# Performance work log

Hardware: AMD Instinct MI355X
Metric: run time of the kernel (lower is better)

## Reference

```python
import jax, jax.numpy as jnp
import numpy as np

N_STK = 32
N_STK_PNT = 64
EMB = 512
BS = 32


def _layer(x, W, scale, bias):
    # Conv2d 1x1 (no bias) + folded BatchNorm2d (eval) + LeakyReLU(0.2)
    # x: [b, c_in, i, j], W: [c_out, c_in]
    h = jnp.einsum('oc,bcij->boij', W, x)
    h = h * scale[None, :, None, None] + bias[None, :, None, None]
    return jax.nn.leaky_relu(h, 0.2)


def setup_inputs() -> dict:
    key = jax.random.key(0)
    ks = jax.random.split(key, 14)
    std = 1.0 / np.sqrt(EMB)
    d = {
        'sparse_fea': jax.random.normal(ks[0], (BS, EMB, N_STK), jnp.float32),
        'dense_fea': jax.random.normal(ks[1], (BS, EMB, N_STK * N_STK_PNT), jnp.float32),
        'Wq': jax.random.normal(ks[2], (EMB, EMB), jnp.float32) * std,
        'sq': jnp.ones((EMB,), jnp.float32),
        'bq': jnp.zeros((EMB,), jnp.float32),
        'Wk': jax.random.normal(ks[3], (EMB, EMB), jnp.float32) * std,
        'sk': jnp.ones((EMB,), jnp.float32),
        'bk': jnp.zeros((EMB,), jnp.float32),
        'Wv': jax.random.normal(ks[4], (EMB, EMB), jnp.float32) * std,
        'sv': jnp.ones((EMB,), jnp.float32),
        'bv': jnp.zeros((EMB,), jnp.float32),
        'Wg': jax.random.normal(ks[5], (EMB, EMB), jnp.float32) * std,
        'sg': jnp.ones((EMB,), jnp.float32),
        'bg': jnp.zeros((EMB,), jnp.float32),
    }
    return d


def reference(sparse_fea, dense_fea, Wq, sq, bq, Wk, sk, bk, Wv, sv, bv, Wg, sg, bg):
    bs, emb, n_pnt = dense_fea.shape
    dense = dense_fea.reshape(bs, emb, N_STK, N_STK_PNT)     # [b, e, s, p]
    sparse = sparse_fea[:, :, :, None]                        # [b, e, s, 1]

    sp_q = _layer(sparse, Wq, sq, bq)                         # [b, E, s, 1]
    dn_k = _layer(dense, Wk, sk, bk)                          # [b, E, s, p]
    sp_v = _layer(sparse, Wv, sv, bv)                         # [b, E, s, 1]

    g = _layer(sp_q - dn_k, Wg, sg, bg)                       # [b, E, s, p]
    coef = jax.nn.softmax(g, axis=1)                          # channel softmax
    out = jnp.sum(coef * sp_v, axis=3)                        # [b, E, s]
    return out
```

## Files before the change

kernel.cpp:

```cpp
#include <hip/hip_runtime.h>
#include <hip/hip_bf16.h>

#define EMB 512
#define NSTK 32
#define NPNT 64
#define BSZ 32

typedef __attribute__((ext_vector_type(8))) _Float16 f16x8;
typedef __attribute__((ext_vector_type(4))) float f32x4;
typedef __attribute__((ext_vector_type(4))) unsigned short us4;
typedef __attribute__((ext_vector_type(8))) unsigned short us8;

static __device__ __forceinline__ unsigned short f16bits(float x) {
    _Float16 h = (_Float16)x;
    return *reinterpret_cast<unsigned short*>(&h);
}

#define GLL(gsrc, ldst)                                                         \
    __builtin_amdgcn_global_load_lds(                                           \
        (const __attribute__((address_space(1))) void*)(gsrc),                  \
        (__attribute__((address_space(3))) void*)(ldst), 16, 0, 0)

#define SBAR() __builtin_amdgcn_s_barrier()

__global__ __launch_bounds__(256)
void prep(const float* __restrict__ wk, const float* __restrict__ wg,
          _Float16* __restrict__ wkf, _Float16* __restrict__ wgf,
          const float* __restrict__ sparse,
          const float* __restrict__ Wq, const float* __restrict__ sq, const float* __restrict__ bq,
          const float* __restrict__ Wv, const float* __restrict__ sv, const float* __restrict__ bv,
          float* __restrict__ outq, float* __restrict__ outv) {
    if (blockIdx.x < 512) {
        int idx = blockIdx.x * blockDim.x + threadIdx.x;
        const float* src;
        _Float16* dst;
        int k;
        if (idx < 65536) { src = wk; dst = wkf; k = idx; }
        else             { src = wg; dst = wgf; k = idx - 65536; }
        f32x4 v = *reinterpret_cast<const f32x4*>(src + (size_t)k * 4);
        us4 o;
#pragma unroll
        for (int e = 0; e < 4; ++e) o[e] = f16bits(v[e]);
        *reinterpret_cast<us4*>(dst + (size_t)k * 4) = o;
        return;
    }

    const int bid = blockIdx.x - 512;
    const int bx = bid & 15, by = (bid >> 4) & 7, bz = bid >> 7;
    const float* W  = (bz == 0) ? Wq : Wv;
    const float* sc = (bz == 0) ? sq : sv;
    const float* bi = (bz == 0) ? bq : bv;
    float* orow     = (bz == 0) ? outq : outv;

    __shared__ float Wt[64][33];
    __shared__ float St[32][65];

    const int m0 = bx * 64;
    const int o0 = by * 64;
    const int t  = threadIdx.x;
    const int ty = t >> 4, tx = t & 15;

    float acc[4][4] = {};

    for (int k0 = 0; k0 < 512; k0 += 32) {
        {
            int ol = t >> 2, kl = (t & 3) * 8;
            const float* p = W + (size_t)(o0 + ol) * 512 + k0 + kl;
            f32x4 v0 = *reinterpret_cast<const f32x4*>(p);
            f32x4 v1 = *reinterpret_cast<const f32x4*>(p + 4);
#pragma unroll
            for (int e = 0; e < 4; ++e) { Wt[ol][kl + e] = v0[e]; Wt[ol][kl + 4 + e] = v1[e]; }
        }
        {
            int kl = t >> 3, ml = (t & 7) * 8;
            int mm = m0 + ml;
            int bb = mm >> 5, iidx = mm & 31;
            const float* p = sparse + (size_t)bb * 16384 + (size_t)(k0 + kl) * 32 + iidx;
            f32x4 v0 = *reinterpret_cast<const f32x4*>(p);
            f32x4 v1 = *reinterpret_cast<const f32x4*>(p + 4);
#pragma unroll
            for (int e = 0; e < 4; ++e) { St[kl][ml + e] = v0[e]; St[kl][ml + 4 + e] = v1[e]; }
        }
        __syncthreads();
#pragma unroll
        for (int kk = 0; kk < 32; ++kk) {
            float av[4], bvv[4];
#pragma unroll
            for (int e = 0; e < 4; ++e) av[e]  = Wt[ty * 4 + e][kk];
#pragma unroll
            for (int e = 0; e < 4; ++e) bvv[e] = St[kk][tx * 4 + e];
#pragma unroll
            for (int a = 0; a < 4; ++a)
#pragma unroll
                for (int bb2 = 0; bb2 < 4; ++bb2) acc[a][bb2] += av[a] * bvv[bb2];
        }
        __syncthreads();
    }
#pragma unroll
    for (int ae = 0; ae < 4; ++ae) {
        int o = o0 + ty * 4 + ae;
        float s = sc[o], bb2 = bi[o];
#pragma unroll
        for (int be = 0; be < 4; ++be) {
            int mm = m0 + tx * 4 + be;
            float h = acc[ae][be] * s + bb2;
            h = (h >= 0.f) ? h : 0.2f * h;
            orow[(size_t)mm * 512 + o] = h;
        }
    }
}

__global__ __launch_bounds__(1024, 4)
void fused_attn(const float* __restrict__ dense,
                const _Float16* __restrict__ wkf,
                const _Float16* __restrict__ wgf,
                const float* __restrict__ wsq,
                const float* __restrict__ wsv,
                const float* __restrict__ sk, const float* __restrict__ bk,
                const float* __restrict__ sg, const float* __restrict__ bg,
                float* __restrict__ out) {
    __shared__ __align__(16) _Float16 XH[64][520];
    __shared__ __align__(16) _Float16 WP[2][512 * 32];
    __shared__ __align__(16) float qrow[512];
    __shared__ __align__(16) float vrow[512];
    __shared__ float wredA[16][64];
    __shared__ float wredB[16][64];

    const int m   = blockIdx.x;
    const int b   = m >> 5, ii = m & 31;
    const int tid = threadIdx.x;
    const int w   = tid >> 6;
    const int l   = tid & 63;
    const int l15 = l & 15;
    const int lk  = l >> 4;

    const int tsw = ((l & 3) - ((l >> 3) & 3)) & 3;
    const int orl = l >> 2;

    {
#pragma unroll
        for (int ih = 0; ih < 2; ++ih) {
            const int o = w * 32 + ih * 16 + orl;
            GLL(wkf + (size_t)o * 512 + tsw * 8,
                &WP[0][(w * 32 + ih * 16) * 32]);
        }
    }

    if (tid < 512) qrow[tid] = wsq[(size_t)m * 512 + tid];
    else           vrow[tid - 512] = wsv[(size_t)m * 512 + (tid - 512)];

    {
        const float* src = dense + (size_t)b * 512 * 2048 + (size_t)ii * 64 + l;
#pragma unroll
        for (int e8 = 0; e8 < 4; ++e8) {
            const int c0 = w * 32 + e8 * 8;
            us8 pk;
#pragma unroll
            for (int e = 0; e < 8; ++e)
                pk[e] = f16bits(src[(size_t)(c0 + e) * 2048]);
            *reinterpret_cast<us8*>(&XH[l][c0]) = pk;
        }
    }
    __syncthreads();

    f32x4 acc[2][4];
#pragma unroll
    for (int fm = 0; fm < 2; ++fm)
#pragma unroll
        for (int fn = 0; fn < 4; ++fn) acc[fm][fn] = (f32x4){0.f, 0.f, 0.f, 0.f};

    const int aslot = (lk + ((l15 >> 1) & 3)) & 3;

    for (int ks = 0; ks < 16; ++ks) {
        {
            const _Float16* wsp = (ks < 15) ? (wkf + (size_t)(ks + 1) * 32) : wgf;
            _Float16* pb = WP[(ks + 1) & 1];
#pragma unroll
            for (int ih = 0; ih < 2; ++ih) {
                const int o = w * 32 + ih * 16 + orl;
                GLL(wsp + (size_t)o * 512 + tsw * 8,
                    pb + (w * 32 + ih * 16) * 32);
            }
        }
        f16x8 bf[4];
#pragma unroll
        for (int fn = 0; fn < 4; ++fn)
            bf[fn] = *reinterpret_cast<const f16x8*>(&XH[fn * 16 + l15][ks * 32 + lk * 8]);
        asm volatile("s_waitcnt vmcnt(2)" ::: "memory");
        {
            const _Float16* pbuf = WP[ks & 1];
            f16x8 af[2];
#pragma unroll
            for (int fm = 0; fm < 2; ++fm)
                af[fm] = *reinterpret_cast<const f16x8*>(
                    pbuf + (w * 32 + fm * 16 + l15) * 32 + aslot * 8);
            __builtin_amdgcn_s_setprio(1);
#pragma unroll
            for (int fm = 0; fm < 2; ++fm)
#pragma unroll
                for (int fn = 0; fn < 4; ++fn)
                    acc[fm][fn] = __builtin_amdgcn_mfma_f32_16x16x32_f16(af[fm], bf[fn], acc[fm][fn], 0, 0, 0);
            __builtin_amdgcn_s_setprio(0);
        }
    }

    asm volatile("s_waitcnt lgkmcnt(0)" ::: "memory");
    SBAR();

#pragma unroll
    for (int fm = 0; fm < 2; ++fm) {
        const int o0 = w * 32 + fm * 16 + lk * 4;
        f32x4 skv = *reinterpret_cast<const f32x4*>(sk + o0);
        f32x4 bkv = *reinterpret_cast<const f32x4*>(bk + o0);
        f32x4 qv4 = *reinterpret_cast<const f32x4*>(&qrow[o0]);
#pragma unroll
        for (int fn = 0; fn < 4; ++fn) {
            const int j = fn * 16 + l15;
            us4 pkh;
#pragma unroll
            for (int r = 0; r < 4; ++r) {
                float h = acc[fm][fn][r] * skv[r] + bkv[r];
                h = (h >= 0.f) ? h : 0.2f * h;
                pkh[r] = f16bits(qv4[r] - h);
            }
            *reinterpret_cast<us4*>(&XH[j][o0]) = pkh;
        }
    }
    asm volatile("s_waitcnt lgkmcnt(0)" ::: "memory");
    SBAR();

#pragma unroll
    for (int fm = 0; fm < 2; ++fm)
#pragma unroll
        for (int fn = 0; fn < 4; ++fn) acc[fm][fn] = (f32x4){0.f, 0.f, 0.f, 0.f};

    for (int ks = 0; ks < 16; ++ks) {
        if (ks < 15) {
            const _Float16* wsp = wgf + (size_t)(ks + 1) * 32;
            _Float16* pb = WP[(ks + 1) & 1];
#pragma unroll
            for (int ih = 0; ih < 2; ++ih) {
                const int o = w * 32 + ih * 16 + orl;
                GLL(wsp + (size_t)o * 512 + tsw * 8,
                    pb + (w * 32 + ih * 16) * 32);
            }
        }
        f16x8 bf[4];
#pragma unroll
        for (int fn = 0; fn < 4; ++fn)
            bf[fn] = *reinterpret_cast<const f16x8*>(&XH[fn * 16 + l15][ks * 32 + lk * 8]);
        if (ks < 15) asm volatile("s_waitcnt vmcnt(2)" ::: "memory");
        else         asm volatile("s_waitcnt vmcnt(0)" ::: "memory");
        {
            const _Float16* pbuf = WP[ks & 1];
            f16x8 af[2];
#pragma unroll
            for (int fm = 0; fm < 2; ++fm)
                af[fm] = *reinterpret_cast<const f16x8*>(
                    pbuf + (w * 32 + fm * 16 + l15) * 32 + aslot * 8);
            __builtin_amdgcn_s_setprio(1);
#pragma unroll
            for (int fm = 0; fm < 2; ++fm)
#pragma unroll
                for (int fn = 0; fn < 4; ++fn)
                    acc[fm][fn] = __builtin_amdgcn_mfma_f32_16x16x32_f16(af[fm], bf[fn], acc[fm][fn], 0, 0, 0);
            __builtin_amdgcn_s_setprio(0);
        }
    }

#pragma unroll
    for (int fm = 0; fm < 2; ++fm) {
        const int o0 = w * 32 + fm * 16 + lk * 4;
        f32x4 sgv = *reinterpret_cast<const f32x4*>(sg + o0);
        f32x4 bgv = *reinterpret_cast<const f32x4*>(bg + o0);
#pragma unroll
        for (int fn = 0; fn < 4; ++fn)
#pragma unroll
            for (int r = 0; r < 4; ++r) {
                float h = acc[fm][fn][r] * sgv[r] + bgv[r];
                acc[fm][fn][r] = (h >= 0.f) ? h : 0.2f * h;
            }
    }

    float pm[4];
#pragma unroll
    for (int fn = 0; fn < 4; ++fn) {
        float mx = -1e30f;
#pragma unroll
        for (int fm = 0; fm < 2; ++fm)
#pragma unroll
            for (int r = 0; r < 4; ++r) mx = fmaxf(mx, acc[fm][fn][r]);
        mx = fmaxf(mx, __shfl_xor(mx, 16, 64));
        mx = fmaxf(mx, __shfl_xor(mx, 32, 64));
        pm[fn] = mx;
    }
    if (l < 16) {
#pragma unroll
        for (int fn = 0; fn < 4; ++fn) wredA[w][fn * 16 + l] = pm[fn];
    }
    __syncthreads();

    float jmax[4];
#pragma unroll
    for (int fn = 0; fn < 4; ++fn) {
        float mx = wredA[0][fn * 16 + l15];
#pragma unroll
        for (int ww = 1; ww < 16; ++ww) mx = fmaxf(mx, wredA[ww][fn * 16 + l15]);
        jmax[fn] = mx;
    }

    float ps[4] = {0.f, 0.f, 0.f, 0.f};
#pragma unroll
    for (int fm = 0; fm < 2; ++fm)
#pragma unroll
        for (int fn = 0; fn < 4; ++fn)
#pragma unroll
            for (int r = 0; r < 4; ++r) {
                float e = __expf(acc[fm][fn][r] - jmax[fn]);
                acc[fm][fn][r] = e;
                ps[fn] += e;
            }
#pragma unroll
    for (int fn = 0; fn < 4; ++fn) {
        ps[fn] += __shfl_xor(ps[fn], 16, 64);
        ps[fn] += __shfl_xor(ps[fn], 32, 64);
    }
    if (l < 16) {
#pragma unroll
        for (int fn = 0; fn < 4; ++fn) wredB[w][fn * 16 + l] = ps[fn];
    }
    __syncthreads();

    float rinv[4];
#pragma unroll
    for (int fn = 0; fn < 4; ++fn) {
        float s = 0.f;
#pragma unroll
        for (int ww = 0; ww < 16; ++ww) s += wredB[ww][fn * 16 + l15];
        rinv[fn] = 1.f / s;
    }

#pragma unroll
    for (int fm = 0; fm < 2; ++fm) {
#pragma unroll
        for (int r = 0; r < 4; ++r) {
            float tsum = 0.f;
#pragma unroll
            for (int fn = 0; fn < 4; ++fn) tsum += acc[fm][fn][r] * rinv[fn];
            tsum += __shfl_xor(tsum, 1, 64);
            tsum += __shfl_xor(tsum, 2, 64);
            tsum += __shfl_xor(tsum, 4, 64);
            tsum += __shfl_xor(tsum, 8, 64);
            if (l15 == 0) {
                int oo = w * 32 + fm * 16 + lk * 4 + r;
                out[((size_t)b * 512 + oo) * 32 + ii] = vrow[oo] * tsum;
            }
        }
    }
}

extern "C" void kernel_launch(void* const* d_in, const int* in_sizes, int n_in,
                              void* d_out, int out_size, void* d_ws, size_t ws_size,
                              hipStream_t stream) {
    const float* sparse = (const float*)d_in[0];
    const float* dense  = (const float*)d_in[1];
    const float* Wq = (const float*)d_in[2];
    const float* sq = (const float*)d_in[3];
    const float* bq = (const float*)d_in[4];
    const float* Wk = (const float*)d_in[5];
    const float* sk = (const float*)d_in[6];
    const float* bk = (const float*)d_in[7];
    const float* Wv = (const float*)d_in[8];
    const float* sv = (const float*)d_in[9];
    const float* bv = (const float*)d_in[10];
    const float* Wg = (const float*)d_in[11];
    const float* sg = (const float*)d_in[12];
    const float* bg = (const float*)d_in[13];
    float* out = (float*)d_out;

    float* wsq = (float*)d_ws;
    float* wsv = wsq + 1024 * 512;
    _Float16* wkf = (_Float16*)(wsv + 1024 * 512);
    _Float16* wgf = wkf + 512 * 512;

    prep<<<768, 256, 0, stream>>>(Wk, Wg, wkf, wgf,
                                  sparse, Wq, sq, bq, Wv, sv, bv, wsq, wsv);
    fused_attn<<<1024, 1024, 0, stream>>>(dense, wkf, wgf, wsq, wsv, sk, bk, sg, bg, out);
}
```

Before: 151.4 us.

## Process four strokes per block and prefetch next stroke's dense tile into registers

Makes each block loop over four consecutive (batch, stroke) items instead of one, and cuts the grid from 1024 to 256 blocks. During the softmax epilogue of one item it loads the next item's dense tile and q/v rows into registers, then writes them to LDS and re-issues the first weight prefetch. The aim is to amortise block launch and prologue cost and to hide the dense-load latency. In exchange there are fewer blocks, which may underfill the GPU's compute units, and more register pressure from the prefetched values.

```diff
diff --git a/kernel.cpp b/kernel.cpp
--- a/kernel.cpp
+++ b/kernel.cpp
@@ -126,8 +126,8 @@
     __shared__ float wredA[16][64];
     __shared__ float wredB[16][64];
 
-    const int m   = blockIdx.x;
-    const int b   = m >> 5, ii = m & 31;
+    const int m0  = blockIdx.x * 4;
+    const int b   = m0 >> 5;
     const int tid = threadIdx.x;
     const int w   = tid >> 6;
     const int l   = tid & 63;
@@ -136,6 +136,7 @@
 
     const int tsw = ((l & 3) - ((l >> 3) & 3)) & 3;
     const int orl = l >> 2;
+    const int aslot = (lk + ((l15 >> 1) & 3)) & 3;
 
     {
 #pragma unroll
@@ -145,12 +146,11 @@
                 &WP[0][(w * 32 + ih * 16) * 32]);
         }
     }
-
-    if (tid < 512) qrow[tid] = wsq[(size_t)m * 512 + tid];
-    else           vrow[tid - 512] = wsv[(size_t)m * 512 + (tid - 512)];
-
+    if (tid < 512) qrow[tid] = wsq[(size_t)m0 * 512 + tid];
+    else           vrow[tid - 512] = wsv[(size_t)m0 * 512 + (tid - 512)];
     {
-        const float* src = dense + (size_t)b * 512 * 2048 + (size_t)ii * 64 + l;
+        const int ii0 = m0 & 31;
+        const float* src = dense + (size_t)b * 512 * 2048 + (size_t)ii0 * 64 + l;
 #pragma unroll
         for (int e8 = 0; e8 < 4; ++e8) {
             const int c0 = w * 32 + e8 * 8;
@@ -163,198 +163,231 @@
     }
     __syncthreads();
 
-    f32x4 acc[2][4];
-#pragma unroll
-    for (int fm = 0; fm < 2; ++fm)
-#pragma unroll
-        for (int fn = 0; fn < 4; ++fn) acc[fm][fn] = (f32x4){0.f, 0.f, 0.f, 0.f};
-
-    const int aslot = (lk + ((l15 >> 1) & 3)) & 3;
-
-    for (int ks = 0; ks < 16; ++ks) {
-        {
-            const _Float16* wsp = (ks < 15) ? (wkf + (size_t)(ks + 1) * 32) : wgf;
-            _Float16* pb = WP[(ks + 1) & 1];
+    for (int rep = 0; rep < 4; ++rep) {
+        const int m  = m0 + rep;
+        const int ii = m & 31;
+
+        f32x4 acc[2][4];
+#pragma unroll
+        for (int fm = 0; fm < 2; ++fm)
+#pragma unroll
+            for (int fn = 0; fn < 4; ++fn) acc[fm][fn] = (f32x4){0.f, 0.f, 0.f, 0.f};
+
+        for (int ks = 0; ks < 16; ++ks) {
+            {
+                const _Float16* wsp = (ks < 15) ? (wkf + (size_t)(ks + 1) * 32) : wgf;
+                _Float16* pb = WP[(ks + 1) & 1];
+#pragma unroll
+                for (int ih = 0; ih < 2; ++ih) {
+                    const int o = w * 32 + ih * 16 + orl;
+                    GLL(wsp + (size_t)o * 512 + tsw * 8, pb + (w * 32 + ih * 16) * 32);
+                }
+            }
+            f16x8 bf[4];
+#pragma unroll
+            for (int fn = 0; fn < 4; ++fn)
+                bf[fn] = *reinterpret_cast<const f16x8*>(&XH[fn * 16 + l15][ks * 32 + lk * 8]);
+            asm volatile("s_waitcnt vmcnt(2)" ::: "memory");
+            {
+                const _Float16* pbuf = WP[ks & 1];
+                f16x8 af[2];
+#pragma unroll
+                for (int fm = 0; fm < 2; ++fm)
+                    af[fm] = *reinterpret_cast<const f16x8*>(
+                        pbuf + (w * 32 + fm * 16 + l15) * 32 + aslot * 8);
+                __builtin_amdgcn_s_setprio(1);
+#pragma unroll
+                for (int fm = 0; fm < 2; ++fm)
+#pragma unroll
+                    for (int fn = 0; fn < 4; ++fn)
+                        acc[fm][fn] = __builtin_amdgcn_mfma_f32_16x16x32_f16(af[fm], bf[fn], acc[fm][fn], 0, 0, 0);
+                __builtin_amdgcn_s_setprio(0);
+            }
+        }
+
+        asm volatile("s_waitcnt lgkmcnt(0)" ::: "memory");
+        SBAR();
+
+#pragma unroll
+        for (int fm = 0; fm < 2; ++fm) {
+            const int o0 = w * 32 + fm * 16 + lk * 4;
+            f32x4 skv = *reinterpret_cast<const f32x4*>(sk + o0);
+            f32x4 bkv = *reinterpret_cast<const f32x4*>(bk + o0);
+            f32x4 qv4 = *reinterpret_cast<const f32x4*>(&qrow[o0]);
+#pragma unroll
+            for (int fn = 0; fn < 4; ++fn) {
+                const int j = fn * 16 + l15;
+                us4 pkh;
+#pragma unroll
+                for (int r = 0; r < 4; ++r) {
+                    float h = acc[fm][fn][r] * skv[r] + bkv[r];
+                    h = (h >= 0.f) ? h : 0.2f * h;
+                    pkh[r] = f16bits(qv4[r] - h);
+                }
+                *reinterpret_cast<us4*>(&XH[j][o0]) = pkh;
+            }
+        }
+        asm volatile("s_waitcnt lgkmcnt(0)" ::: "memory");
+        SBAR();
+
+#pragma unroll
+        for (int fm = 0; fm < 2; ++fm)
+#pragma unroll
+            for (int fn = 0; fn < 4; ++fn) acc[fm][fn] = (f32x4){0.f, 0.f, 0.f, 0.f};
+
+        for (int ks = 0; ks < 16; ++ks) {
+            if (ks < 15) {
+                const _Float16* wsp = wgf + (size_t)(ks + 1) * 32;
+                _Float16* pb = WP[(ks + 1) & 1];
+#pragma unroll
+                for (int ih = 0; ih < 2; ++ih) {
+                    const int o = w * 32 + ih * 16 + orl;
+                    GLL(wsp + (size_t)o * 512 + tsw * 8, pb + (w * 32 + ih * 16) * 32);
+                }
+            }
+            f16x8 bf[4];
+#pragma unroll
+            for (int fn = 0; fn < 4; ++fn)
+                bf[fn] = *reinterpret_cast<const f16x8*>(&XH[fn * 16 + l15][ks * 32 + lk * 8]);
+            if (ks < 15) asm volatile("s_waitcnt vmcnt(2)" ::: "memory");
+            else         asm volatile("s_waitcnt vmcnt(0)" ::: "memory");
+            {
+                const _Float16* pbuf = WP[ks & 1];
+                f16x8 af[2];
+#pragma unroll
+                for (int fm = 0; fm < 2; ++fm)
+                    af[fm] = *reinterpret_cast<const f16x8*>(
+                        pbuf + (w * 32 + fm * 16 + l15) * 32 + aslot * 8);
+                __builtin_amdgcn_s_setprio(1);
+#pragma unroll
+                for (int fm = 0; fm < 2; ++fm)
+#pragma unroll
+                    for (int fn = 0; fn < 4; ++fn)
+                        acc[fm][fn] = __builtin_amdgcn_mfma_f32_16x16x32_f16(af[fm], bf[fn], acc[fm][fn], 0, 0, 0);
+                __builtin_amdgcn_s_setprio(0);
+            }
+        }
+
+        us8 xpk[4];
+        float qn = 0.f, vn = 0.f;
+        const bool more = (rep < 3);
+        if (more) {
+            const int iin = (m + 1) & 31;
+            const float* srcn = dense + (size_t)b * 512 * 2048 + (size_t)iin * 64 + l;
+#pragma unroll
+            for (int e8 = 0; e8 < 4; ++e8) {
+#pragma unroll
+                for (int e = 0; e < 8; ++e)
+                    xpk[e8][e] = f16bits(srcn[(size_t)(w * 32 + e8 * 8 + e) * 2048]);
+            }
+            if (tid < 512) qn = wsq[(size_t)(m + 1) * 512 + tid];
+            else           vn = wsv[(size_t)(m + 1) * 512 + (tid - 512)];
+        }
+
+#pragma unroll
+        for (int fm = 0; fm < 2; ++fm) {
+            const int o0 = w * 32 + fm * 16 + lk * 4;
+            f32x4 sgv = *reinterpret_cast<const f32x4*>(sg + o0);
+            f32x4 bgv = *reinterpret_cast<const f32x4*>(bg + o0);
+#pragma unroll
+            for (int fn = 0; fn < 4; ++fn)
+#pragma unroll
+                for (int r = 0; r < 4; ++r) {
+                    float h = acc[fm][fn][r] * sgv[r] + bgv[r];
+                    acc[fm][fn][r] = (h >= 0.f) ? h : 0.2f * h;
+                }
+        }
+
+        float pm[4];
+#pragma unroll
+        for (int fn = 0; fn < 4; ++fn) {
+            float mx = -1e30f;
+#pragma unroll
+            for (int fm = 0; fm < 2; ++fm)
+#pragma unroll
+                for (int r = 0; r < 4; ++r) mx = fmaxf(mx, acc[fm][fn][r]);
+            mx = fmaxf(mx, __shfl_xor(mx, 16, 64));
+            mx = fmaxf(mx, __shfl_xor(mx, 32, 64));
+            pm[fn] = mx;
+        }
+        if (l < 16) {
+#pragma unroll
+            for (int fn = 0; fn < 4; ++fn) wredA[w][fn * 16 + l] = pm[fn];
+        }
+        __syncthreads();
+
+        float jmax[4];
+#pragma unroll
+        for (int fn = 0; fn < 4; ++fn) {
+            float mx = wredA[0][fn * 16 + l15];
+#pragma unroll
+            for (int ww = 1; ww < 16; ++ww) mx = fmaxf(mx, wredA[ww][fn * 16 + l15]);
+            jmax[fn] = mx;
+        }
+
+        float ps[4] = {0.f, 0.f, 0.f, 0.f};
+#pragma unroll
+        for (int fm = 0; fm < 2; ++fm)
+#pragma unroll
+            for (int fn = 0; fn < 4; ++fn)
+#pragma unroll
+                for (int r = 0; r < 4; ++r) {
+                    float e = __expf(acc[fm][fn][r] - jmax[fn]);
+                    acc[fm][fn][r] = e;
+                    ps[fn] += e;
+                }
+#pragma unroll
+        for (int fn = 0; fn < 4; ++fn) {
+            ps[fn] += __shfl_xor(ps[fn], 16, 64);
+            ps[fn] += __shfl_xor(ps[fn], 32, 64);
+        }
+        if (l < 16) {
+#pragma unroll
+            for (int fn = 0; fn < 4; ++fn) wredB[w][fn * 16 + l] = ps[fn];
+        }
+        __syncthreads();
+
+        float rinv[4];
+#pragma unroll
+        for (int fn = 0; fn < 4; ++fn) {
+            float s = 0.f;
+#pragma unroll
+            for (int ww = 0; ww < 16; ++ww) s += wredB[ww][fn * 16 + l15];
+            rinv[fn] = 1.f / s;
+        }
+
+#pragma unroll
+        for (int fm = 0; fm < 2; ++fm) {
+#pragma unroll
+            for (int r = 0; r < 4; ++r) {
+                float tsum = 0.f;
+#pragma unroll
+                for (int fn = 0; fn < 4; ++fn) tsum += acc[fm][fn][r] * rinv[fn];
+                tsum += __shfl_xor(tsum, 1, 64);
+                tsum += __shfl_xor(tsum, 2, 64);
+                tsum += __shfl_xor(tsum, 4, 64);
+                tsum += __shfl_xor(tsum, 8, 64);
+                if (l15 == 0) {
+                    int oo = w * 32 + fm * 16 + lk * 4 + r;
+                    out[((size_t)b * 512 + oo) * 32 + ii] = vrow[oo] * tsum;
+                }
+            }
+        }
+
+        if (more) {
+            SBAR();
+#pragma unroll
+            for (int e8 = 0; e8 < 4; ++e8)
+                *reinterpret_cast<us8*>(&XH[l][w * 32 + e8 * 8]) = xpk[e8];
+            if (tid < 512) qrow[tid] = qn;
+            else           vrow[tid - 512] = vn;
 #pragma unroll
             for (int ih = 0; ih < 2; ++ih) {
                 const int o = w * 32 + ih * 16 + orl;
-                GLL(wsp + (size_t)o * 512 + tsw * 8,
-                    pb + (w * 32 + ih * 16) * 32);
-            }
-        }
-        f16x8 bf[4];
-#pragma unroll
-        for (int fn = 0; fn < 4; ++fn)
-            bf[fn] = *reinterpret_cast<const f16x8*>(&XH[fn * 16 + l15][ks * 32 + lk * 8]);
-        asm volatile("s_waitcnt vmcnt(2)" ::: "memory");
-        {
-            const _Float16* pbuf = WP[ks & 1];
-            f16x8 af[2];
-#pragma unroll
-            for (int fm = 0; fm < 2; ++fm)
-                af[fm] = *reinterpret_cast<const f16x8*>(
-                    pbuf + (w * 32 + fm * 16 + l15) * 32 + aslot * 8);
-            __builtin_amdgcn_s_setprio(1);
-#pragma unroll
-            for (int fm = 0; fm < 2; ++fm)
-#pragma unroll
-                for (int fn = 0; fn < 4; ++fn)
-                    acc[fm][fn] = __builtin_amdgcn_mfma_f32_16x16x32_f16(af[fm], bf[fn], acc[fm][fn], 0, 0, 0);
-            __builtin_amdgcn_s_setprio(0);
-        }
-    }
-
-    asm volatile("s_waitcnt lgkmcnt(0)" ::: "memory");
-    SBAR();
-
-#pragma unroll
-    for (int fm = 0; fm < 2; ++fm) {
-        const int o0 = w * 32 + fm * 16 + lk * 4;
-        f32x4 skv = *reinterpret_cast<const f32x4*>(sk + o0);
-        f32x4 bkv = *reinterpret_cast<const f32x4*>(bk + o0);
-        f32x4 qv4 = *reinterpret_cast<const f32x4*>(&qrow[o0]);
-#pragma unroll
-        for (int fn = 0; fn < 4; ++fn) {
-            const int j = fn * 16 + l15;
-            us4 pkh;
-#pragma unroll
-            for (int r = 0; r < 4; ++r) {
-                float h = acc[fm][fn][r] * skv[r] + bkv[r];
-                h = (h >= 0.f) ? h : 0.2f * h;
-                pkh[r] = f16bits(qv4[r] - h);
-            }
-            *reinterpret_cast<us4*>(&XH[j][o0]) = pkh;
-        }
-    }
-    asm volatile("s_waitcnt lgkmcnt(0)" ::: "memory");
-    SBAR();
-
-#pragma unroll
-    for (int fm = 0; fm < 2; ++fm)
-#pragma unroll
-        for (int fn = 0; fn < 4; ++fn) acc[fm][fn] = (f32x4){0.f, 0.f, 0.f, 0.f};
-
-    for (int ks = 0; ks < 16; ++ks) {
-        if (ks < 15) {
-            const _Float16* wsp = wgf + (size_t)(ks + 1) * 32;
-            _Float16* pb = WP[(ks + 1) & 1];
-#pragma unroll
-            for (int ih = 0; ih < 2; ++ih) {
-                const int o = w * 32 + ih * 16 + orl;
-                GLL(wsp + (size_t)o * 512 + tsw * 8,
-                    pb + (w * 32 + ih * 16) * 32);
-            }
-        }
-        f16x8 bf[4];
-#pragma unroll
-        for (int fn = 0; fn < 4; ++fn)
-            bf[fn] = *reinterpret_cast<const f16x8*>(&XH[fn * 16 + l15][ks * 32 + lk * 8]);
-        if (ks < 15) asm volatile("s_waitcnt vmcnt(2)" ::: "memory");
-        else         asm volatile("s_waitcnt vmcnt(0)" ::: "memory");
-        {
-            const _Float16* pbuf = WP[ks & 1];
-            f16x8 af[2];
-#pragma unroll
-            for (int fm = 0; fm < 2; ++fm)
-                af[fm] = *reinterpret_cast<const f16x8*>(
-                    pbuf + (w * 32 + fm * 16 + l15) * 32 + aslot * 8);
-            __builtin_amdgcn_s_setprio(1);
-#pragma unroll
-            for (int fm = 0; fm < 2; ++fm)
-#pragma unroll
-                for (int fn = 0; fn < 4; ++fn)
-                    acc[fm][fn] = __builtin_amdgcn_mfma_f32_16x16x32_f16(af[fm], bf[fn], acc[fm][fn], 0, 0, 0);
-            __builtin_amdgcn_s_setprio(0);
-        }
-    }
-
-#pragma unroll
-    for (int fm = 0; fm < 2; ++fm) {
-        const int o0 = w * 32 + fm * 16 + lk * 4;
-        f32x4 sgv = *reinterpret_cast<const f32x4*>(sg + o0);
-        f32x4 bgv = *reinterpret_cast<const f32x4*>(bg + o0);
-#pragma unroll
-        for (int fn = 0; fn < 4; ++fn)
-#pragma unroll
-            for (int r = 0; r < 4; ++r) {
-                float h = acc[fm][fn][r] * sgv[r] + bgv[r];
-                acc[fm][fn][r] = (h >= 0.f) ? h : 0.2f * h;
-            }
-    }
-
-    float pm[4];
-#pragma unroll
-    for (int fn = 0; fn < 4; ++fn) {
-        float mx = -1e30f;
-#pragma unroll
-        for (int fm = 0; fm < 2; ++fm)
-#pragma unroll
-            for (int r = 0; r < 4; ++r) mx = fmaxf(mx, acc[fm][fn][r]);
-        mx = fmaxf(mx, __shfl_xor(mx, 16, 64));
-        mx = fmaxf(mx, __shfl_xor(mx, 32, 64));
-        pm[fn] = mx;
-    }
-    if (l < 16) {
-#pragma unroll
-        for (int fn = 0; fn < 4; ++fn) wredA[w][fn * 16 + l] = pm[fn];
-    }
-    __syncthreads();
-
-    float jmax[4];
-#pragma unroll
-    for (int fn = 0; fn < 4; ++fn) {
-        float mx = wredA[0][fn * 16 + l15];
-#pragma unroll
-        for (int ww = 1; ww < 16; ++ww) mx = fmaxf(mx, wredA[ww][fn * 16 + l15]);
-        jmax[fn] = mx;
-    }
-
-    float ps[4] = {0.f, 0.f, 0.f, 0.f};
-#pragma unroll
-    for (int fm = 0; fm < 2; ++fm)
-#pragma unroll
-        for (int fn = 0; fn < 4; ++fn)
-#pragma unroll
-            for (int r = 0; r < 4; ++r) {
-                float e = __expf(acc[fm][fn][r] - jmax[fn]);
-                acc[fm][fn][r] = e;
-                ps[fn] += e;
-            }
-#pragma unroll
-    for (int fn = 0; fn < 4; ++fn) {
-        ps[fn] += __shfl_xor(ps[fn], 16, 64);
-        ps[fn] += __shfl_xor(ps[fn], 32, 64);
-    }
-    if (l < 16) {
-#pragma unroll
-        for (int fn = 0; fn < 4; ++fn) wredB[w][fn * 16 + l] = ps[fn];
-    }
-    __syncthreads();
-
-    float rinv[4];
-#pragma unroll
-    for (int fn = 0; fn < 4; ++fn) {
-        float s = 0.f;
-#pragma unroll
-        for (int ww = 0; ww < 16; ++ww) s += wredB[ww][fn * 16 + l15];
-        rinv[fn] = 1.f / s;
-    }
-
-#pragma unroll
-    for (int fm = 0; fm < 2; ++fm) {
-#pragma unroll
-        for (int r = 0; r < 4; ++r) {
-            float tsum = 0.f;
-#pragma unroll
-            for (int fn = 0; fn < 4; ++fn) tsum += acc[fm][fn][r] * rinv[fn];
-            tsum += __shfl_xor(tsum, 1, 64);
-            tsum += __shfl_xor(tsum, 2, 64);
-            tsum += __shfl_xor(tsum, 4, 64);
-            tsum += __shfl_xor(tsum, 8, 64);
-            if (l15 == 0) {
-                int oo = w * 32 + fm * 16 + lk * 4 + r;
-                out[((size_t)b * 512 + oo) * 32 + ii] = vrow[oo] * tsum;
-            }
+                GLL(wkf + (size_t)o * 512 + tsw * 8,
+                    &WP[0][(w * 32 + ih * 16) * 32]);
+            }
+            __syncthreads();
         }
     }
 }
@@ -385,5 +418,5 @@
 
     prep<<<768, 256, 0, stream>>>(Wk, Wg, wkf, wgf,
                                   sparse, Wq, sq, bq, Wv, sv, bv, wsq, wsv);
-    fused_attn<<<1024, 1024, 0, stream>>>(dense, wkf, wgf, wsq, wsv, sk, bk, sg, bg, out);
+    fused_attn<<<256, 1024, 0, stream>>>(dense, wkf, wgf, wsq, wsv, sk, bk, sg, bg, out);
 }
```

Result: slower. 338.1 us (+123.3%).

## Software-pipeline LDS fragment loads one k-step ahead of MFMAs

Applied to the files above, without the earlier changes.

Restructures both GEMM k-loops so weight tiles are prefetched two steps ahead into the double buffer, and the A/B register fragments for step k+1 are loaded from LDS while the MFMAs for step k run. The aim is to hide LDS read latency behind matrix math instead of stalling before each MFMA group. In exchange it uses more registers for the extra fragments and changes the buffer indexing. Each wave relies only on its own lgkmcnt and vmcnt waits, with no block barrier inside the loop, so correctness depends on each wave reading and writing only its own rows of the weight buffer.

```diff
diff --git a/kernel.cpp b/kernel.cpp
--- a/kernel.cpp
+++ b/kernel.cpp
@@ -136,14 +136,12 @@
 
     const int tsw = ((l & 3) - ((l >> 3) & 3)) & 3;
     const int orl = l >> 2;
-
-    {
-#pragma unroll
-        for (int ih = 0; ih < 2; ++ih) {
-            const int o = w * 32 + ih * 16 + orl;
-            GLL(wkf + (size_t)o * 512 + tsw * 8,
-                &WP[0][(w * 32 + ih * 16) * 32]);
-        }
+    const int aslot = (lk + ((l15 >> 1) & 3)) & 3;
+
+#pragma unroll
+    for (int ih = 0; ih < 2; ++ih) {
+        const int o = w * 32 + ih * 16 + orl;
+        GLL(wkf + (size_t)o * 512 + tsw * 8, &WP[0][(w * 32 + ih * 16) * 32]);
     }
 
     if (tid < 512) qrow[tid] = wsq[(size_t)m * 512 + tid];
@@ -169,39 +167,57 @@
 #pragma unroll
         for (int fn = 0; fn < 4; ++fn) acc[fm][fn] = (f32x4){0.f, 0.f, 0.f, 0.f};
 
-    const int aslot = (lk + ((l15 >> 1) & 3)) & 3;
+    f16x8 af[2], bf[4], afn[2], bfn[4];
+
+#pragma unroll
+    for (int ih = 0; ih < 2; ++ih) {
+        const int o = w * 32 + ih * 16 + orl;
+        GLL(wkf + (size_t)o * 512 + 32 + tsw * 8, &WP[1][(w * 32 + ih * 16) * 32]);
+    }
+#pragma unroll
+    for (int fm = 0; fm < 2; ++fm)
+        af[fm] = *reinterpret_cast<const f16x8*>(
+            &WP[0][(w * 32 + fm * 16 + l15) * 32 + aslot * 8]);
+#pragma unroll
+    for (int fn = 0; fn < 4; ++fn)
+        bf[fn] = *reinterpret_cast<const f16x8*>(&XH[fn * 16 + l15][lk * 8]);
 
     for (int ks = 0; ks < 16; ++ks) {
+        asm volatile("s_waitcnt lgkmcnt(0)" ::: "memory");
         {
-            const _Float16* wsp = (ks < 15) ? (wkf + (size_t)(ks + 1) * 32) : wgf;
-            _Float16* pb = WP[(ks + 1) & 1];
+            const _Float16* nxt = (ks <= 13) ? (wkf + (size_t)(ks + 2) * 32)
+                                : (ks == 14) ? wgf : (wgf + 32);
 #pragma unroll
             for (int ih = 0; ih < 2; ++ih) {
                 const int o = w * 32 + ih * 16 + orl;
-                GLL(wsp + (size_t)o * 512 + tsw * 8,
-                    pb + (w * 32 + ih * 16) * 32);
-            }
-        }
-        f16x8 bf[4];
-#pragma unroll
-        for (int fn = 0; fn < 4; ++fn)
-            bf[fn] = *reinterpret_cast<const f16x8*>(&XH[fn * 16 + l15][ks * 32 + lk * 8]);
+                GLL(nxt + (size_t)o * 512 + tsw * 8, &WP[ks & 1][(w * 32 + ih * 16) * 32]);
+            }
+        }
         asm volatile("s_waitcnt vmcnt(2)" ::: "memory");
         {
-            const _Float16* pbuf = WP[ks & 1];
-            f16x8 af[2];
+            const _Float16* pbuf = WP[(ks + 1) & 1];
 #pragma unroll
             for (int fm = 0; fm < 2; ++fm)
-                af[fm] = *reinterpret_cast<const f16x8*>(
+                afn[fm] = *reinterpret_cast<const f16x8*>(
                     pbuf + (w * 32 + fm * 16 + l15) * 32 + aslot * 8);
-            __builtin_amdgcn_s_setprio(1);
-#pragma unroll
-            for (int fm = 0; fm < 2; ++fm)
+            if (ks < 15) {
 #pragma unroll
                 for (int fn = 0; fn < 4; ++fn)
-                    acc[fm][fn] = __builtin_amdgcn_mfma_f32_16x16x32_f16(af[fm], bf[fn], acc[fm][fn], 0, 0, 0);
-            __builtin_amdgcn_s_setprio(0);
-        }
+                    bfn[fn] = *reinterpret_cast<const f16x8*>(
+                        &XH[fn * 16 + l15][(ks + 1) * 32 + lk * 8]);
+            }
+        }
+        __builtin_amdgcn_s_setprio(1);
+#pragma unroll
+        for (int fm = 0; fm < 2; ++fm)
+#pragma unroll
+            for (int fn = 0; fn < 4; ++fn)
+                acc[fm][fn] = __builtin_amdgcn_mfma_f32_16x16x32_f16(af[fm], bf[fn], acc[fm][fn], 0, 0, 0);
+        __builtin_amdgcn_s_setprio(0);
+#pragma unroll
+        for (int fm = 0; fm < 2; ++fm) af[fm] = afn[fm];
+#pragma unroll
+        for (int fn = 0; fn < 4; ++fn) bf[fn] = bfn[fn];
     }
 
     asm volatile("s_waitcnt lgkmcnt(0)" ::: "memory");
@@ -234,37 +250,46 @@
 #pragma unroll
         for (int fn = 0; fn < 4; ++fn) acc[fm][fn] = (f32x4){0.f, 0.f, 0.f, 0.f};
 
-    for (int ks = 0; ks < 16; ++ks) {
-        if (ks < 15) {
-            const _Float16* wsp = wgf + (size_t)(ks + 1) * 32;
-            _Float16* pb = WP[(ks + 1) & 1];
+#pragma unroll
+    for (int fn = 0; fn < 4; ++fn)
+        bf[fn] = *reinterpret_cast<const f16x8*>(&XH[fn * 16 + l15][lk * 8]);
+
+    for (int g = 0; g < 16; ++g) {
+        asm volatile("s_waitcnt lgkmcnt(0)" ::: "memory");
+        if (g <= 13) {
+            const _Float16* nxt = wgf + (size_t)(g + 2) * 32;
 #pragma unroll
             for (int ih = 0; ih < 2; ++ih) {
                 const int o = w * 32 + ih * 16 + orl;
-                GLL(wsp + (size_t)o * 512 + tsw * 8,
-                    pb + (w * 32 + ih * 16) * 32);
-            }
-        }
-        f16x8 bf[4];
-#pragma unroll
-        for (int fn = 0; fn < 4; ++fn)
-            bf[fn] = *reinterpret_cast<const f16x8*>(&XH[fn * 16 + l15][ks * 32 + lk * 8]);
-        if (ks < 15) asm volatile("s_waitcnt vmcnt(2)" ::: "memory");
-        else         asm volatile("s_waitcnt vmcnt(0)" ::: "memory");
-        {
-            const _Float16* pbuf = WP[ks & 1];
-            f16x8 af[2];
+                GLL(nxt + (size_t)o * 512 + tsw * 8, &WP[g & 1][(w * 32 + ih * 16) * 32]);
+            }
+            asm volatile("s_waitcnt vmcnt(2)" ::: "memory");
+        } else {
+            asm volatile("s_waitcnt vmcnt(0)" ::: "memory");
+        }
+        if (g < 15) {
+            const _Float16* pbuf = WP[(g + 1) & 1];
 #pragma unroll
             for (int fm = 0; fm < 2; ++fm)
-                af[fm] = *reinterpret_cast<const f16x8*>(
+                afn[fm] = *reinterpret_cast<const f16x8*>(
                     pbuf + (w * 32 + fm * 16 + l15) * 32 + aslot * 8);
-            __builtin_amdgcn_s_setprio(1);
-#pragma unroll
-            for (int fm = 0; fm < 2; ++fm)
-#pragma unroll
-                for (int fn = 0; fn < 4; ++fn)
-                    acc[fm][fn] = __builtin_amdgcn_mfma_f32_16x16x32_f16(af[fm], bf[fn], acc[fm][fn], 0, 0, 0);
-            __builtin_amdgcn_s_setprio(0);
+#pragma unroll
+            for (int fn = 0; fn < 4; ++fn)
+                bfn[fn] = *reinterpret_cast<const f16x8*>(
+                    &XH[fn * 16 + l15][(g + 1) * 32 + lk * 8]);
+        }
+        __builtin_amdgcn_s_setprio(1);
+#pragma unroll
+        for (int fm = 0; fm < 2; ++fm)
+#pragma unroll
+            for (int fn = 0; fn < 4; ++fn)
+                acc[fm][fn] = __builtin_amdgcn_mfma_f32_16x16x32_f16(af[fm], bf[fn], acc[fm][fn], 0, 0, 0);
+        __builtin_amdgcn_s_setprio(0);
+        if (g < 15) {
+#pragma unroll
+            for (int fm = 0; fm < 2; ++fm) af[fm] = afn[fm];
+#pragma unroll
+            for (int fn = 0; fn < 4; ++fn) bf[fn] = bfn[fn];
         }
     }
 
```

Measured after the change: 151.3 us, median of 3. No clear change (-0.1%).

## Software-pipeline LDS fragment loads with register double-buffering and deeper weight prefetch

Applied to the files above, without the earlier changes.

Both GEMM loops are fully unrolled into macros that load the next k-step's A and B fragments from LDS into a second register set while the MFMAs of the current step run. The global-to-LDS weight prefetch now runs two steps ahead instead of one, and LDS reads use inline ds_read_b128 on precomputed addresses. The intent is to hide LDS and global latency behind MFMA work. In exchange, register pressure rises from the doubled fragments at 1024 threads per block, and the ordering relies on hand-placed waitcnt and sched_barrier, which is fragile with no explicit block barriers between the LDS-DMA writes and the reads.

```diff
diff --git a/kernel.cpp b/kernel.cpp
--- a/kernel.cpp
+++ b/kernel.cpp
@@ -22,6 +22,12 @@
         (__attribute__((address_space(3))) void*)(ldst), 16, 0, 0)
 
 #define SBAR() __builtin_amdgcn_s_barrier()
+
+static __device__ __forceinline__ unsigned ldsaddr(void* p) {
+    return (unsigned)(unsigned long long)(__attribute__((address_space(3))) void*)p;
+}
+
+#define DSR(dst, a) asm volatile("ds_read_b128 %0, %1" : "=v"(dst) : "v"(a))
 
 __global__ __launch_bounds__(256)
 void prep(const float* __restrict__ wk, const float* __restrict__ wg,
@@ -110,6 +116,78 @@
     }
 }
 
+
+#define G1_ITER(IT, AM, BM, AN, BN)                                             \
+    {                                                                           \
+        asm volatile("s_waitcnt lgkmcnt(0)" ::: "memory");                      \
+        __builtin_amdgcn_sched_barrier(0);                                      \
+        const _Float16* nxt = (IT <= 13) ? (wkf + (size_t)(IT + 2) * 32)        \
+                            : (IT == 14) ? wgf : (wgf + 32);                    \
+        _Pragma("unroll")                                                       \
+        for (int ih = 0; ih < 2; ++ih) {                                        \
+            const int o = w * 32 + ih * 16 + orl;                               \
+            GLL(nxt + (size_t)o * 512 + tsw * 8,                                \
+                &WP[IT & 1][(w * 32 + ih * 16) * 32]);                          \
+        }                                                                       \
+        asm volatile("s_waitcnt vmcnt(2)" ::: "memory");                        \
+        {                                                                       \
+            const unsigned ab = (((IT + 1) & 1) ? wpb1 : wpb0) + af_off;        \
+            DSR(AN[0], ab);                                                     \
+            DSR(AN[1], ab + 1024u);                                             \
+            if (IT < 15) {                                                      \
+                const unsigned bb = bf_base + (unsigned)((IT + 1) * 64);        \
+                DSR(BN[0], bb);                                                 \
+                DSR(BN[1], bb + 16640u);                                        \
+                DSR(BN[2], bb + 33280u);                                        \
+                DSR(BN[3], bb + 49920u);                                        \
+            }                                                                   \
+        }                                                                       \
+        __builtin_amdgcn_s_setprio(1);                                          \
+        _Pragma("unroll")                                                       \
+        for (int fm = 0; fm < 2; ++fm)                                          \
+            _Pragma("unroll")                                                   \
+            for (int fn = 0; fn < 4; ++fn)                                      \
+                acc[fm][fn] = __builtin_amdgcn_mfma_f32_16x16x32_f16(           \
+                    AM[fm], BM[fn], acc[fm][fn], 0, 0, 0);                      \
+        __builtin_amdgcn_s_setprio(0);                                          \
+    }
+
+#define G2_ITER(IT, AM, BM, AN, BN)                                             \
+    {                                                                           \
+        asm volatile("s_waitcnt lgkmcnt(0)" ::: "memory");                      \
+        __builtin_amdgcn_sched_barrier(0);                                      \
+        if (IT <= 13) {                                                         \
+            const _Float16* nxt = wgf + (size_t)(IT + 2) * 32;                  \
+            _Pragma("unroll")                                                   \
+            for (int ih = 0; ih < 2; ++ih) {                                    \
+                const int o = w * 32 + ih * 16 + orl;                           \
+                GLL(nxt + (size_t)o * 512 + tsw * 8,                            \
+                    &WP[IT & 1][(w * 32 + ih * 16) * 32]);                      \
+            }                                                                   \
+            asm volatile("s_waitcnt vmcnt(2)" ::: "memory");                    \
+        } else {                                                                \
+            asm volatile("s_waitcnt vmcnt(0)" ::: "memory");                    \
+        }                                                                       \
+        if (IT < 15) {                                                          \
+            const unsigned ab = (((IT + 1) & 1) ? wpb1 : wpb0) + af_off;        \
+            DSR(AN[0], ab);                                                     \
+            DSR(AN[1], ab + 1024u);                                             \
+            const unsigned bb = bf_base + (unsigned)((IT + 1) * 64);            \
+            DSR(BN[0], bb);                                                     \
+            DSR(BN[1], bb + 16640u);                                            \
+            DSR(BN[2], bb + 33280u);                                            \
+            DSR(BN[3], bb + 49920u);                                            \
+        }                                                                       \
+        __builtin_amdgcn_s_setprio(1);                                          \
+        _Pragma("unroll")                                                       \
+        for (int fm = 0; fm < 2; ++fm)                                          \
+            _Pragma("unroll")                                                   \
+            for (int fn = 0; fn < 4; ++fn)                                      \
+                acc[fm][fn] = __builtin_amdgcn_mfma_f32_16x16x32_f16(           \
+                    AM[fm], BM[fn], acc[fm][fn], 0, 0, 0);                      \
+        __builtin_amdgcn_s_setprio(0);                                          \
+    }
+
 __global__ __launch_bounds__(1024, 4)
 void fused_attn(const float* __restrict__ dense,
                 const _Float16* __restrict__ wkf,
@@ -136,14 +214,18 @@
 
     const int tsw = ((l & 3) - ((l >> 3) & 3)) & 3;
     const int orl = l >> 2;
-
-    {
-#pragma unroll
-        for (int ih = 0; ih < 2; ++ih) {
-            const int o = w * 32 + ih * 16 + orl;
-            GLL(wkf + (size_t)o * 512 + tsw * 8,
-                &WP[0][(w * 32 + ih * 16) * 32]);
-        }
+    const int aslot = (lk + ((l15 >> 1) & 3)) & 3;
+
+    const unsigned xh_base = ldsaddr(&XH[0][0]);
+    const unsigned wpb0    = ldsaddr(&WP[0][0]);
+    const unsigned wpb1    = ldsaddr(&WP[1][0]);
+    const unsigned bf_base = xh_base + (unsigned)(l15 * 1040 + lk * 16);
+    const unsigned af_off  = (unsigned)((w * 32 + l15) * 64 + aslot * 16);
+
+#pragma unroll
+    for (int ih = 0; ih < 2; ++ih) {
+        const int o = w * 32 + ih * 16 + orl;
+        GLL(wkf + (size_t)o * 512 + tsw * 8, &WP[0][(w * 32 + ih * 16) * 32]);
     }
 
     if (tid < 512) qrow[tid] = wsq[(size_t)m * 512 + tid];
@@ -169,40 +251,39 @@
 #pragma unroll
         for (int fn = 0; fn < 4; ++fn) acc[fm][fn] = (f32x4){0.f, 0.f, 0.f, 0.f};
 
-    const int aslot = (lk + ((l15 >> 1) & 3)) & 3;
-
-    for (int ks = 0; ks < 16; ++ks) {
-        {
-            const _Float16* wsp = (ks < 15) ? (wkf + (size_t)(ks + 1) * 32) : wgf;
-            _Float16* pb = WP[(ks + 1) & 1];
-#pragma unroll
-            for (int ih = 0; ih < 2; ++ih) {
-                const int o = w * 32 + ih * 16 + orl;
-                GLL(wsp + (size_t)o * 512 + tsw * 8,
-                    pb + (w * 32 + ih * 16) * 32);
-            }
-        }
-        f16x8 bf[4];
-#pragma unroll
-        for (int fn = 0; fn < 4; ++fn)
-            bf[fn] = *reinterpret_cast<const f16x8*>(&XH[fn * 16 + l15][ks * 32 + lk * 8]);
-        asm volatile("s_waitcnt vmcnt(2)" ::: "memory");
-        {
-            const _Float16* pbuf = WP[ks & 1];
-            f16x8 af[2];
-#pragma unroll
-            for (int fm = 0; fm < 2; ++fm)
-                af[fm] = *reinterpret_cast<const f16x8*>(
-                    pbuf + (w * 32 + fm * 16 + l15) * 32 + aslot * 8);
-            __builtin_amdgcn_s_setprio(1);
-#pragma unroll
-            for (int fm = 0; fm < 2; ++fm)
-#pragma unroll
-                for (int fn = 0; fn < 4; ++fn)
-                    acc[fm][fn] = __builtin_amdgcn_mfma_f32_16x16x32_f16(af[fm], bf[fn], acc[fm][fn], 0, 0, 0);
-            __builtin_amdgcn_s_setprio(0);
-        }
-    }
+    f16x8 afA[2], bfA[4], afB[2], bfB[4];
+
+#pragma unroll
+    for (int ih = 0; ih < 2; ++ih) {
+        const int o = w * 32 + ih * 16 + orl;
+        GLL(wkf + (size_t)o * 512 + 32 + tsw * 8, &WP[1][(w * 32 + ih * 16) * 32]);
+    }
+    {
+        const unsigned ab = wpb0 + af_off;
+        DSR(afA[0], ab);
+        DSR(afA[1], ab + 1024u);
+        DSR(bfA[0], bf_base);
+        DSR(bfA[1], bf_base + 16640u);
+        DSR(bfA[2], bf_base + 33280u);
+        DSR(bfA[3], bf_base + 49920u);
+    }
+
+    G1_ITER(0,  afA, bfA, afB, bfB)
+    G1_ITER(1,  afB, bfB, afA, bfA)
+    G1_ITER(2,  afA, bfA, afB, bfB)
+    G1_ITER(3,  afB, bfB, afA, bfA)
+    G1_ITER(4,  afA, bfA, afB, bfB)
+    G1_ITER(5,  afB, bfB, afA, bfA)
+    G1_ITER(6,  afA, bfA, afB, bfB)
+    G1_ITER(7,  afB, bfB, afA, bfA)
+    G1_ITER(8,  afA, bfA, afB, bfB)
+    G1_ITER(9,  afB, bfB, afA, bfA)
+    G1_ITER(10, afA, bfA, afB, bfB)
+    G1_ITER(11, afB, bfB, afA, bfA)
+    G1_ITER(12, afA, bfA, afB, bfB)
+    G1_ITER(13, afB, bfB, afA, bfA)
+    G1_ITER(14, afA, bfA, afB, bfB)
+    G1_ITER(15, afB, bfB, afA, bfA)
 
     asm volatile("s_waitcnt lgkmcnt(0)" ::: "memory");
     SBAR();
@@ -234,39 +315,27 @@
 #pragma unroll
         for (int fn = 0; fn < 4; ++fn) acc[fm][fn] = (f32x4){0.f, 0.f, 0.f, 0.f};
 
-    for (int ks = 0; ks < 16; ++ks) {
-        if (ks < 15) {
-            const _Float16* wsp = wgf + (size_t)(ks + 1) * 32;
-            _Float16* pb = WP[(ks + 1) & 1];
-#pragma unroll
-            for (int ih = 0; ih < 2; ++ih) {
-                const int o = w * 32 + ih * 16 + orl;
-                GLL(wsp + (size_t)o * 512 + tsw * 8,
-                    pb + (w * 32 + ih * 16) * 32);
-            }
-        }
-        f16x8 bf[4];
-#pragma unroll
-        for (int fn = 0; fn < 4; ++fn)
-            bf[fn] = *reinterpret_cast<const f16x8*>(&XH[fn * 16 + l15][ks * 32 + lk * 8]);
-        if (ks < 15) asm volatile("s_waitcnt vmcnt(2)" ::: "memory");
-        else         asm volatile("s_waitcnt vmcnt(0)" ::: "memory");
-        {
-            const _Float16* pbuf = WP[ks & 1];
-            f16x8 af[2];
-#pragma unroll
-            for (int fm = 0; fm < 2; ++fm)
-                af[fm] = *reinterpret_cast<const f16x8*>(
-                    pbuf + (w * 32 + fm * 16 + l15) * 32 + aslot * 8);
-            __builtin_amdgcn_s_setprio(1);
-#pragma unroll
-            for (int fm = 0; fm < 2; ++fm)
-#pragma unroll
-                for (int fn = 0; fn < 4; ++fn)
-                    acc[fm][fn] = __builtin_amdgcn_mfma_f32_16x16x32_f16(af[fm], bf[fn], acc[fm][fn], 0, 0, 0);
-            __builtin_amdgcn_s_setprio(0);
-        }
-    }
+    DSR(bfA[0], bf_base);
+    DSR(bfA[1], bf_base + 16640u);
+    DSR(bfA[2], bf_base + 33280u);
+    DSR(bfA[3], bf_base + 49920u);
+
+    G2_ITER(0,  afA, bfA, afB, bfB)
+    G2_ITER(1,  afB, bfB, afA, bfA)
+    G2_ITER(2,  afA, bfA, afB, bfB)
+    G2_ITER(3,  afB, bfB, afA, bfA)
+    G2_ITER(4,  afA, bfA, afB, bfB)
+    G2_ITER(5,  afB, bfB, afA, bfA)
+    G2_ITER(6,  afA, bfA, afB, bfB)
+    G2_ITER(7,  afB, bfB, afA, bfA)
+    G2_ITER(8,  afA, bfA, afB, bfB)
+    G2_ITER(9,  afB, bfB, afA, bfA)
+    G2_ITER(10, afA, bfA, afB, bfB)
+    G2_ITER(11, afB, bfB, afA, bfA)
+    G2_ITER(12, afA, bfA, afB, bfB)
+    G2_ITER(13, afB, bfB, afA, bfA)
+    G2_ITER(14, afA, bfA, afB, bfB)
+    G2_ITER(15, afB, bfB, afA, bfA)
 
 #pragma unroll
     for (int fm = 0; fm < 2; ++fm) {
```

Measured after the change: 196.7 us. 29.9% more time.
